# Performance work log

Measured on AMD Instinct MI355X. Metric: run time of the kernel, lower is better.

Reference implementation:

```python
import jax, jax.numpy as jnp
import numpy as np

B, L, D = 4, 2048, 512
H = 8
DK = 512 // H  # 64
DV = 512 // H  # 64
TEMP = float(np.power(DK, 0.5))
LN_EPS = 1e-5


def setup_inputs() -> dict:
    key = jax.random.key(0)
    ks = jax.random.split(key, 12)
    s = 0.02
    return {
        "q": jax.random.normal(ks[0], (B, L, D), jnp.float32),
        "k": jax.random.normal(ks[1], (B, L, D), jnp.float32),
        "v": jax.random.normal(ks[2], (B, L, D), jnp.float32),
        "mask": jax.random.randint(ks[3], (B, L, L), 0, 2, jnp.int32),
        "wq_w": jax.random.normal(ks[4], (H * DK, D), jnp.float32) * s,
        "wq_b": jnp.zeros((H * DK,), jnp.float32),
        "wv_w": jax.random.normal(ks[5], (H * DV, D), jnp.float32) * s,
        "wv_b": jnp.zeros((H * DV,), jnp.float32),
        "fc_w": jax.random.normal(ks[6], (D, H * DV), jnp.float32) * s,
        "fc_b": jnp.zeros((D,), jnp.float32),
        "ln_g": jnp.ones((D,), jnp.float32),
        "ln_b": jnp.zeros((D,), jnp.float32),
    }


def reference(q, k, v, mask, wq_w, wq_b, wv_w, wv_b, fc_w, fc_b, ln_g, ln_b):
    residual = q
    # NOTE: source module projects k with w_qs (bug preserved faithfully)
    qh = (q @ wq_w.T + wq_b).reshape(B, L, H, DK).transpose(0, 2, 1, 3)  # bhld
    kh = (k @ wq_w.T + wq_b).reshape(B, L, H, DK).transpose(0, 2, 1, 3)
    vh = (v @ wv_w.T + wv_b).reshape(B, L, H, DV).transpose(0, 2, 1, 3)
    attn = jnp.einsum("bhqd,bhkd->bhqk", qh / TEMP, kh)
    attn = jnp.where(mask[:, None, :, :] == 1, -1e9, attn)
    attn = jax.nn.softmax(attn, axis=-1)
    out = jnp.einsum("bhqk,bhkd->bhqd", attn, vh)  # (B, H, L, DV)
    # faithful buffer reinterpretation: .view(n_head, sz_b, L, DV)
    out = out.reshape(H, B, L, DV).transpose(0, 2, 1, 3).reshape(B, L, H * DV)
    out = out @ fc_w.T + fc_b
    x = out + residual
    mu = jnp.mean(x, axis=-1, keepdims=True)
    var = jnp.mean(jnp.square(x - mu), axis=-1, keepdims=True)
    y = (x - mu) / jnp.sqrt(var + LN_EPS) * ln_g + ln_b
    return (y, attn)
```

## Files before the change

kernel.cpp:

```cpp
#include <hip/hip_runtime.h>

#define NB 4
#define NL 2048
#define ND 512
#define NH 8
#define NTOK (NB * NL)

constexpr float LN_EPS = 1e-5f;

typedef __attribute__((ext_vector_type(8))) short bf16x8;
typedef __attribute__((ext_vector_type(4))) float f32x4;

static __device__ __forceinline__ unsigned short f2bf(float f) {
  unsigned u = __builtin_bit_cast(unsigned, f);
  unsigned r = (u + 0x7fffu + ((u >> 16) & 1u)) >> 16;
  return (unsigned short)r;
}

static __device__ __forceinline__ uint2 pk4(const float4 f) {
  uint2 r;
  r.x = (unsigned)f2bf(f.x) | ((unsigned)f2bf(f.y) << 16);
  r.y = (unsigned)f2bf(f.z) | ((unsigned)f2bf(f.w) << 16);
  return r;
}

#define MFMA_GEMM_PRELUDE                                                      \
  __shared__ unsigned short As[64 * 72];                                       \
  __shared__ unsigned short Bs[64 * 72];                                       \
  const int tid = threadIdx.x;                                                 \
  const int w = tid >> 6;                                                      \
  const int lane = tid & 63;                                                   \
  const int quad = lane >> 4, l15 = lane & 15;                                 \
  const int m0 = blockIdx.x * 64, n0 = blockIdx.y * 64;                        \
  const int srow = tid >> 2;                                                   \
  const int c4 = (tid & 3) * 4;                                                \
  const int scol = (tid & 3) * 16;                                             \
  f32x4 acc[4];                                                                \
  acc[0] = acc[1] = acc[2] = acc[3] = (f32x4){0.f, 0.f, 0.f, 0.f};

#define MFMA_STEP(AV, BV)                                                      \
  do {                                                                         \
    __syncthreads();                                                           \
    _Pragma("unroll") for (int j = 0; j < 4; ++j) {                            \
      *(uint2*)&As[srow * 72 + c4 + j * 16] = pk4(AV[j]);                      \
      *(uint2*)&Bs[srow * 72 + c4 + j * 16] = pk4(BV[j]);                      \
    }                                                                          \
    __syncthreads();                                                           \
    _Pragma("unroll") for (int ks = 0; ks < 2; ++ks) {                         \
      const bf16x8 af = *(const bf16x8*)&As[(w * 16 + l15) * 72 + ks * 32 + quad * 8]; \
      _Pragma("unroll") for (int nt = 0; nt < 4; ++nt) {                       \
        const bf16x8 bfr = *(const bf16x8*)&Bs[(nt * 16 + l15) * 72 + ks * 32 + quad * 8]; \
        acc[nt] = __builtin_amdgcn_mfma_f32_16x16x32_bf16(af, bfr, acc[nt], 0, 0, 0); \
      }                                                                        \
    }                                                                          \
  } while (0)

__global__ __launch_bounds__(256) void gemm_qk_mfma(const float* __restrict__ X,
                                                    const float* __restrict__ W,
                                                    const float* __restrict__ bias,
                                                    unsigned short* __restrict__ out,
                                                    float scale) {
  MFMA_GEMM_PRELUDE
  for (int k0 = 0; k0 < 512; k0 += 64) {
    float4 av[4], bv[4];
#pragma unroll
    for (int j = 0; j < 4; ++j) {
      av[j] = *(const float4*)&X[(size_t)(m0 + srow) * ND + k0 + c4 + j * 16];
      bv[j] = *(const float4*)&W[(size_t)(n0 + srow) * ND + k0 + c4 + j * 16];
    }
    MFMA_STEP(av, bv);
  }
  const int hh = n0 >> 6;
  __syncthreads();
#pragma unroll
  for (int nt = 0; nt < 4; ++nt) {
    const float b = bias[n0 + nt * 16 + l15];
#pragma unroll
    for (int r = 0; r < 4; ++r)
      As[(w * 16 + quad * 4 + r) * 72 + nt * 16 + l15] = f2bf((acc[nt][r] + b) * scale);
  }
  __syncthreads();
  const int tok = m0 + srow;
  const int bb = tok >> 11, l = tok & 2047;
  unsigned short* orow = out + (((size_t)bb * NH + hh) * NL + l) * 64;
  *(uint4*)&orow[scol] = *(const uint4*)&As[srow * 72 + scol];
  *(uint4*)&orow[scol + 8] = *(const uint4*)&As[srow * 72 + scol + 8];
}

__global__ __launch_bounds__(256) void gemm_v_mfma_t(const float* __restrict__ X,
                                                     const float* __restrict__ W,
                                                     const float* __restrict__ bias,
                                                     unsigned short* __restrict__ outT) {
  MFMA_GEMM_PRELUDE
  for (int k0 = 0; k0 < 512; k0 += 64) {
    float4 av[4], bv[4];
#pragma unroll
    for (int j = 0; j < 4; ++j) {
      av[j] = *(const float4*)&X[(size_t)(m0 + srow) * ND + k0 + c4 + j * 16];
      bv[j] = *(const float4*)&W[(size_t)(n0 + srow) * ND + k0 + c4 + j * 16];
    }
    MFMA_STEP(av, bv);
  }
  const int hh = n0 >> 6;
  __syncthreads();
#pragma unroll
  for (int nt = 0; nt < 4; ++nt) {
    const float b = bias[n0 + nt * 16 + l15];
#pragma unroll
    for (int r = 0; r < 4; ++r)
      As[(nt * 16 + l15) * 72 + w * 16 + quad * 4 + r] = f2bf(acc[nt][r] + b);
  }
  __syncthreads();
  const int bb = m0 >> 11, l0 = m0 & 2047;
  unsigned short* orow = outT + (((size_t)bb * NH + hh) * 64 + srow) * NL + l0;
  *(uint4*)&orow[scol] = *(const uint4*)&As[srow * 72 + scol];
  *(uint4*)&orow[scol + 8] = *(const uint4*)&As[srow * 72 + scol + 8];
}

__global__ __launch_bounds__(256) void attn_mfma(const unsigned short* __restrict__ qh,
                                                 const unsigned short* __restrict__ kh,
                                                 const unsigned short* __restrict__ vT,
                                                 const int* __restrict__ mask,
                                                 float* __restrict__ attn,
                                                 float* __restrict__ ao) {
  const int b = blockIdx.z, h = blockIdx.y, q0 = blockIdx.x * 64;
  const int bh = b * NH + h;
  __shared__ unsigned short Ks[64 * 72];
  __shared__ unsigned short Vt[64 * 72];
  __shared__ unsigned short Ps[4 * 16 * 72];
  const int tid = threadIdx.x;
  const int w = tid >> 6, lane = tid & 63;
  const int quad = lane >> 4, l15 = lane & 15;

  const size_t qoff = ((size_t)bh * NL + q0 + w * 16 + l15) * 64 + quad * 8;
  const bf16x8 aq0 = *(const bf16x8*)(qh + qoff);
  const bf16x8 aq1 = *(const bf16x8*)(qh + qoff + 32);

  const int srow = tid >> 2;
  const int scol = (tid & 3) * 16;

  float rinv[4] = {0.f, 0.f, 0.f, 0.f};
  unsigned int mbits[16];
#pragma unroll
  for (int i = 0; i < 16; ++i) mbits[i] = 0;

  for (int kt = 0; kt < 32; ++kt) {
    const unsigned short* kg = kh + ((size_t)bh * NL + kt * 64 + srow) * 64 + scol;
    const uint4 k0 = *(const uint4*)kg;
    const uint4 k1 = *(const uint4*)(kg + 8);
    __syncthreads();
    *(uint4*)&Ks[srow * 72 + scol] = k0;
    *(uint4*)&Ks[srow * 72 + scol + 8] = k1;
    __syncthreads();
    f32x4 s[4];
#pragma unroll
    for (int nt = 0; nt < 4; ++nt) {
      const bf16x8 b0 = *(const bf16x8*)&Ks[(nt * 16 + l15) * 72 + quad * 8];
      const bf16x8 b1 = *(const bf16x8*)&Ks[(nt * 16 + l15) * 72 + 32 + quad * 8];
      f32x4 acc = {0.f, 0.f, 0.f, 0.f};
      acc = __builtin_amdgcn_mfma_f32_16x16x32_bf16(aq0, b0, acc, 0, 0, 0);
      acc = __builtin_amdgcn_mfma_f32_16x16x32_bf16(aq1, b1, acc, 0, 0, 0);
      s[nt] = acc;
    }
    unsigned int mb = 0;
#pragma unroll
    for (int r = 0; r < 4; ++r) {
      const size_t mrow = ((size_t)b * NL + q0 + w * 16 + quad * 4 + r) * NL + kt * 64;
#pragma unroll
      for (int nt = 0; nt < 4; ++nt) {
        const int mz = mask[mrow + nt * 16 + l15];
        float e = __expf(s[nt][r]);
        if (mz == 1) {
          mb |= (1u << (nt * 4 + r));
          e = 0.f;
        }
        rinv[r] += e;
      }
    }
    mbits[kt >> 1] |= mb << ((kt & 1) * 16);
  }
#pragma unroll
  for (int r = 0; r < 4; ++r) {
    float v = rinv[r];
    v += __shfl_xor(v, 1);
    v += __shfl_xor(v, 2);
    v += __shfl_xor(v, 4);
    v += __shfl_xor(v, 8);
    rinv[r] = 1.0f / v;
  }

  f32x4 oacc[4];
#pragma unroll
  for (int nt = 0; nt < 4; ++nt) oacc[nt] = (f32x4){0.f, 0.f, 0.f, 0.f};

  for (int kt = 0; kt < 32; ++kt) {
    const unsigned short* kg = kh + ((size_t)bh * NL + kt * 64 + srow) * 64 + scol;
    const unsigned short* vg = vT + ((size_t)bh * 64 + srow) * NL + kt * 64 + scol;
    const uint4 k0 = *(const uint4*)kg;
    const uint4 k1 = *(const uint4*)(kg + 8);
    const uint4 v0 = *(const uint4*)vg;
    const uint4 v1 = *(const uint4*)(vg + 8);
    __syncthreads();
    *(uint4*)&Ks[srow * 72 + scol] = k0;
    *(uint4*)&Ks[srow * 72 + scol + 8] = k1;
    *(uint4*)&Vt[srow * 72 + scol] = v0;
    *(uint4*)&Vt[srow * 72 + scol + 8] = v1;
    __syncthreads();
    f32x4 s[4];
#pragma unroll
    for (int nt = 0; nt < 4; ++nt) {
      const bf16x8 b0 = *(const bf16x8*)&Ks[(nt * 16 + l15) * 72 + quad * 8];
      const bf16x8 b1 = *(const bf16x8*)&Ks[(nt * 16 + l15) * 72 + 32 + quad * 8];
      f32x4 acc = {0.f, 0.f, 0.f, 0.f};
      acc = __builtin_amdgcn_mfma_f32_16x16x32_bf16(aq0, b0, acc, 0, 0, 0);
      acc = __builtin_amdgcn_mfma_f32_16x16x32_bf16(aq1, b1, acc, 0, 0, 0);
      s[nt] = acc;
    }
    const unsigned int mb = mbits[kt >> 1] >> ((kt & 1) * 16);
#pragma unroll
    for (int r = 0; r < 4; ++r) {
      const int q = q0 + w * 16 + quad * 4 + r;
      float* arow = attn + ((size_t)bh * NL + q) * NL + kt * 64;
      unsigned short* prow = &Ps[(w * 16 + quad * 4 + r) * 72];
#pragma unroll
      for (int nt = 0; nt < 4; ++nt) {
        float e = ((mb >> (nt * 4 + r)) & 1u) ? 0.f : __expf(s[nt][r]) * rinv[r];
        arow[nt * 16 + l15] = e;
        prow[nt * 16 + l15] = f2bf(e);
      }
    }
    const bf16x8 pa0 = *(const bf16x8*)&Ps[(w * 16 + l15) * 72 + quad * 8];
    const bf16x8 pa1 = *(const bf16x8*)&Ps[(w * 16 + l15) * 72 + 32 + quad * 8];
#pragma unroll
    for (int nt = 0; nt < 4; ++nt) {
      const bf16x8 vb0 = *(const bf16x8*)&Vt[(nt * 16 + l15) * 72 + quad * 8];
      const bf16x8 vb1 = *(const bf16x8*)&Vt[(nt * 16 + l15) * 72 + 32 + quad * 8];
      oacc[nt] = __builtin_amdgcn_mfma_f32_16x16x32_bf16(pa0, vb0, oacc[nt], 0, 0, 0);
      oacc[nt] = __builtin_amdgcn_mfma_f32_16x16x32_bf16(pa1, vb1, oacc[nt], 0, 0, 0);
    }
  }
#pragma unroll
  for (int r = 0; r < 4; ++r) {
    float* orow = ao + ((size_t)bh * NL + q0 + w * 16 + quad * 4 + r) * 64;
#pragma unroll
    for (int nt = 0; nt < 4; ++nt) orow[nt * 16 + l15] = oacc[nt][r];
  }
}

__global__ __launch_bounds__(256) void fc_gather_mfma(const float* __restrict__ AO,
                                                      const float* __restrict__ W,
                                                      const float* __restrict__ bias,
                                                      const float* __restrict__ resid,
                                                      float* __restrict__ Xout) {
  MFMA_GEMM_PRELUDE
  const int nrow = m0 + srow;
  const int b_out = nrow >> 11;
  const int l_out = nrow & 2047;
  const int h2 = b_out * 2 + (l_out >> 10);
  const int q2base = (l_out & 1023) << 1;
  for (int k0 = 0; k0 < 512; k0 += 64) {
    const int q2 = q2base | ((k0 >> 8) & 1);
    const int b2 = (k0 >> 6) & 3;
    const float* abase = AO + ((size_t)(h2 * 4 + b2) * NL + q2) * 64;
    float4 av[4], bv[4];
#pragma unroll
    for (int j = 0; j < 4; ++j) {
      av[j] = *(const float4*)&abase[c4 + j * 16];
      bv[j] = *(const float4*)&W[(size_t)(n0 + srow) * ND + k0 + c4 + j * 16];
    }
    MFMA_STEP(av, bv);
  }
#pragma unroll
  for (int nt = 0; nt < 4; ++nt) {
    const float b = bias[n0 + nt * 16 + l15];
#pragma unroll
    for (int r = 0; r < 4; ++r) {
      const int row = m0 + w * 16 + quad * 4 + r;
      const float rv = resid[(size_t)row * ND + n0 + nt * 16 + l15];
      Xout[(size_t)row * ND + n0 + nt * 16 + l15] = acc[nt][r] + b + rv;
    }
  }
}

__global__ __launch_bounds__(64) void layernorm_k(const float* __restrict__ x,
                                                  const float* __restrict__ g,
                                                  const float* __restrict__ bta,
                                                  float* __restrict__ y) {
  const int n = blockIdx.x;
  const int lane = threadIdx.x;
  const float* row = x + (size_t)n * ND;
  const float4 a = *(const float4*)&row[lane * 8];
  const float4 c = *(const float4*)&row[lane * 8 + 4];
  float s = a.x + a.y + a.z + a.w + c.x + c.y + c.z + c.w;
  float sq = a.x * a.x + a.y * a.y + a.z * a.z + a.w * a.w +
             c.x * c.x + c.y * c.y + c.z * c.z + c.w * c.w;
#pragma unroll
  for (int off = 32; off; off >>= 1) {
    s += __shfl_down(s, off);
    sq += __shfl_down(sq, off);
  }
  s = __shfl(s, 0);
  sq = __shfl(sq, 0);
  const float mu = s * (1.f / 512.f);
  const float var = sq * (1.f / 512.f) - mu * mu;
  const float rstd = rsqrtf(var + LN_EPS);
  float* yo = y + (size_t)n * ND;
  const int c0 = lane * 8;
  float4 o1, o2;
  o1.x = (a.x - mu) * rstd * g[c0 + 0] + bta[c0 + 0];
  o1.y = (a.y - mu) * rstd * g[c0 + 1] + bta[c0 + 1];
  o1.z = (a.z - mu) * rstd * g[c0 + 2] + bta[c0 + 2];
  o1.w = (a.w - mu) * rstd * g[c0 + 3] + bta[c0 + 3];
  o2.x = (c.x - mu) * rstd * g[c0 + 4] + bta[c0 + 4];
  o2.y = (c.y - mu) * rstd * g[c0 + 5] + bta[c0 + 5];
  o2.z = (c.z - mu) * rstd * g[c0 + 6] + bta[c0 + 6];
  o2.w = (c.w - mu) * rstd * g[c0 + 7] + bta[c0 + 7];
  *(float4*)&yo[c0] = o1;
  *(float4*)&yo[c0 + 4] = o2;
}

extern "C" void kernel_launch(void* const* d_in, const int* in_sizes, int n_in,
                              void* d_out, int out_size, void* d_ws, size_t ws_size,
                              hipStream_t stream) {
  const float* q = (const float*)d_in[0];
  const float* k = (const float*)d_in[1];
  const float* v = (const float*)d_in[2];
  const int* mask = (const int*)d_in[3];
  const float* wq_w = (const float*)d_in[4];
  const float* wq_b = (const float*)d_in[5];
  const float* wv_w = (const float*)d_in[6];
  const float* wv_b = (const float*)d_in[7];
  const float* fc_w = (const float*)d_in[8];
  const float* fc_b = (const float*)d_in[9];
  const float* ln_g = (const float*)d_in[10];
  const float* ln_b = (const float*)d_in[11];

  float* y = (float*)d_out;
  float* attn = y + (size_t)NTOK * ND;

  const size_t SZ = (size_t)NTOK * ND;
  unsigned short* qhb = (unsigned short*)d_ws;
  unsigned short* khb = qhb + SZ;
  unsigned short* vTb = khb + SZ;
  float* ao = (float*)(vTb + SZ);
  float* xx = ao + SZ;

  const dim3 gproj(NTOK / 64, ND / 64);
  gemm_qk_mfma<<<gproj, 256, 0, stream>>>(q, wq_w, wq_b, qhb, 0.125f);
  gemm_qk_mfma<<<gproj, 256, 0, stream>>>(k, wq_w, wq_b, khb, 1.0f);
  gemm_v_mfma_t<<<gproj, 256, 0, stream>>>(v, wv_w, wv_b, vTb);
  attn_mfma<<<dim3(NL / 64, NH, NB), 256, 0, stream>>>(qhb, khb, vTb, mask, attn, ao);
  fc_gather_mfma<<<gproj, 256, 0, stream>>>(ao, fc_w, fc_b, q, xx);
  layernorm_k<<<NTOK, 64, 0, stream>>>(xx, ln_g, ln_b, y);
}
```

Measured before the change: 870.4 us.

## Pre-convert inputs and weights to bf16, bit-pack mask, store attention output as bf16

Adds a pre-pass that converts q/k/v and the three weight matrices to bf16, so the projection and fc GEMMs load bf16 directly instead of converting fp32 per tile. The int32 mask is packed into 64-bit ballot words once, so the attention kernel reads one 64-bit word per row per key tile rather than 64 int32 values. The attention output is also written as bf16 through shared memory with vectorized stores. The extra conversion kernels cost an additional read and write pass over the inputs, which may offset the savings.

```diff
diff --git a/kernel.cpp b/kernel.cpp
--- a/kernel.cpp
+++ b/kernel.cpp
@@ -24,7 +24,33 @@
   return r;
 }
 
-#define MFMA_GEMM_PRELUDE                                                      \
+__global__ __launch_bounds__(256) void cvt3_bf16(const float* __restrict__ s0,
+                                                 const float* __restrict__ s1,
+                                                 const float* __restrict__ s2,
+                                                 unsigned short* __restrict__ d0,
+                                                 unsigned short* __restrict__ d1,
+                                                 unsigned short* __restrict__ d2) {
+  const float* s = (blockIdx.y == 0) ? s0 : (blockIdx.y == 1) ? s1 : s2;
+  unsigned short* d = (blockIdx.y == 0) ? d0 : (blockIdx.y == 1) ? d1 : d2;
+  const size_t i = ((size_t)blockIdx.x * 256 + threadIdx.x) * 8;
+  const float4 a = *(const float4*)&s[i];
+  const float4 b = *(const float4*)&s[i + 4];
+  uint4 o;
+  const uint2 lo = pk4(a), hi = pk4(b);
+  o.x = lo.x; o.y = lo.y; o.z = hi.x; o.w = hi.y;
+  *(uint4*)&d[i] = o;
+}
+
+__global__ __launch_bounds__(256) void pack_mask(const int* __restrict__ mask,
+                                                 unsigned long long* __restrict__ mpk) {
+  const int w = threadIdx.x >> 6, lane = threadIdx.x & 63;
+  const size_t g = (size_t)blockIdx.x * 4 + w;
+  const int m = mask[g * 64 + lane];
+  const unsigned long long bits = __ballot(m == 1);
+  if (lane == 0) mpk[g] = bits;
+}
+
+#define BF16_GEMM_PRELUDE                                                      \
   __shared__ unsigned short As[64 * 72];                                       \
   __shared__ unsigned short Bs[64 * 72];                                       \
   const int tid = threadIdx.x;                                                 \
@@ -33,18 +59,21 @@
   const int quad = lane >> 4, l15 = lane & 15;                                 \
   const int m0 = blockIdx.x * 64, n0 = blockIdx.y * 64;                        \
   const int srow = tid >> 2;                                                   \
-  const int c4 = (tid & 3) * 4;                                                \
   const int scol = (tid & 3) * 16;                                             \
   f32x4 acc[4];                                                                \
   acc[0] = acc[1] = acc[2] = acc[3] = (f32x4){0.f, 0.f, 0.f, 0.f};
 
-#define MFMA_STEP(AV, BV)                                                      \
+#define BF16_GEMM_STEP(ap, bp)                                                 \
   do {                                                                         \
+    const uint4 a0 = *(const uint4*)((ap));                                    \
+    const uint4 a1 = *(const uint4*)((ap) + 8);                                \
+    const uint4 b0 = *(const uint4*)((bp));                                    \
+    const uint4 b1 = *(const uint4*)((bp) + 8);                                \
     __syncthreads();                                                           \
-    _Pragma("unroll") for (int j = 0; j < 4; ++j) {                            \
-      *(uint2*)&As[srow * 72 + c4 + j * 16] = pk4(AV[j]);                      \
-      *(uint2*)&Bs[srow * 72 + c4 + j * 16] = pk4(BV[j]);                      \
-    }                                                                          \
+    *(uint4*)&As[srow * 72 + scol] = a0;                                       \
+    *(uint4*)&As[srow * 72 + scol + 8] = a1;                                   \
+    *(uint4*)&Bs[srow * 72 + scol] = b0;                                       \
+    *(uint4*)&Bs[srow * 72 + scol + 8] = b1;                                   \
     __syncthreads();                                                           \
     _Pragma("unroll") for (int ks = 0; ks < 2; ++ks) {                         \
       const bf16x8 af = *(const bf16x8*)&As[(w * 16 + l15) * 72 + ks * 32 + quad * 8]; \
@@ -55,20 +84,16 @@
     }                                                                          \
   } while (0)
 
-__global__ __launch_bounds__(256) void gemm_qk_mfma(const float* __restrict__ X,
-                                                    const float* __restrict__ W,
+__global__ __launch_bounds__(256) void gemm_qk_mfma(const unsigned short* __restrict__ X,
+                                                    const unsigned short* __restrict__ W,
                                                     const float* __restrict__ bias,
                                                     unsigned short* __restrict__ out,
                                                     float scale) {
-  MFMA_GEMM_PRELUDE
+  BF16_GEMM_PRELUDE
   for (int k0 = 0; k0 < 512; k0 += 64) {
-    float4 av[4], bv[4];
-#pragma unroll
-    for (int j = 0; j < 4; ++j) {
-      av[j] = *(const float4*)&X[(size_t)(m0 + srow) * ND + k0 + c4 + j * 16];
-      bv[j] = *(const float4*)&W[(size_t)(n0 + srow) * ND + k0 + c4 + j * 16];
-    }
-    MFMA_STEP(av, bv);
+    const unsigned short* ap = X + (size_t)(m0 + srow) * ND + k0 + scol;
+    const unsigned short* bp = W + (size_t)(n0 + srow) * ND + k0 + scol;
+    BF16_GEMM_STEP(ap, bp);
   }
   const int hh = n0 >> 6;
   __syncthreads();
@@ -87,19 +112,15 @@
   *(uint4*)&orow[scol + 8] = *(const uint4*)&As[srow * 72 + scol + 8];
 }
 
-__global__ __launch_bounds__(256) void gemm_v_mfma_t(const float* __restrict__ X,
-                                                     const float* __restrict__ W,
+__global__ __launch_bounds__(256) void gemm_v_mfma_t(const unsigned short* __restrict__ X,
+                                                     const unsigned short* __restrict__ W,
                                                      const float* __restrict__ bias,
                                                      unsigned short* __restrict__ outT) {
-  MFMA_GEMM_PRELUDE
+  BF16_GEMM_PRELUDE
   for (int k0 = 0; k0 < 512; k0 += 64) {
-    float4 av[4], bv[4];
-#pragma unroll
-    for (int j = 0; j < 4; ++j) {
-      av[j] = *(const float4*)&X[(size_t)(m0 + srow) * ND + k0 + c4 + j * 16];
-      bv[j] = *(const float4*)&W[(size_t)(n0 + srow) * ND + k0 + c4 + j * 16];
-    }
-    MFMA_STEP(av, bv);
+    const unsigned short* ap = X + (size_t)(m0 + srow) * ND + k0 + scol;
+    const unsigned short* bp = W + (size_t)(n0 + srow) * ND + k0 + scol;
+    BF16_GEMM_STEP(ap, bp);
   }
   const int hh = n0 >> 6;
   __syncthreads();
@@ -120,9 +141,9 @@
 __global__ __launch_bounds__(256) void attn_mfma(const unsigned short* __restrict__ qh,
                                                  const unsigned short* __restrict__ kh,
                                                  const unsigned short* __restrict__ vT,
-                                                 const int* __restrict__ mask,
+                                                 const unsigned long long* __restrict__ mpk,
                                                  float* __restrict__ attn,
-                                                 float* __restrict__ ao) {
+                                                 unsigned short* __restrict__ ao) {
   const int b = blockIdx.z, h = blockIdx.y, q0 = blockIdx.x * 64;
   const int bh = b * NH + h;
   __shared__ unsigned short Ks[64 * 72];
@@ -139,6 +160,8 @@
   const int srow = tid >> 2;
   const int scol = (tid & 3) * 16;
 
+  const size_t mrowq = ((size_t)b * NL + q0 + w * 16 + quad * 4) * 32;
+
   float rinv[4] = {0.f, 0.f, 0.f, 0.f};
   unsigned int mbits[16];
 #pragma unroll
@@ -148,6 +171,9 @@
     const unsigned short* kg = kh + ((size_t)bh * NL + kt * 64 + srow) * 64 + scol;
     const uint4 k0 = *(const uint4*)kg;
     const uint4 k1 = *(const uint4*)(kg + 8);
+    unsigned long long mq[4];
+#pragma unroll
+    for (int r = 0; r < 4; ++r) mq[r] = mpk[mrowq + (size_t)r * 32 + kt];
     __syncthreads();
     *(uint4*)&Ks[srow * 72 + scol] = k0;
     *(uint4*)&Ks[srow * 72 + scol + 8] = k1;
@@ -165,15 +191,17 @@
     unsigned int mb = 0;
 #pragma unroll
     for (int r = 0; r < 4; ++r) {
-      const size_t mrow = ((size_t)b * NL + q0 + w * 16 + quad * 4 + r) * NL + kt * 64;
+      const unsigned long long t = mq[r] >> l15;
+      mb |= ((unsigned)t & 1u) << (0 + r);
+      mb |= (((unsigned)t >> 16) & 1u) << (4 + r);
+      mb |= (((unsigned)(t >> 32)) & 1u) << (8 + r);
+      mb |= (((unsigned)(t >> 48)) & 1u) << (12 + r);
+    }
+#pragma unroll
+    for (int r = 0; r < 4; ++r) {
 #pragma unroll
       for (int nt = 0; nt < 4; ++nt) {
-        const int mz = mask[mrow + nt * 16 + l15];
-        float e = __expf(s[nt][r]);
-        if (mz == 1) {
-          mb |= (1u << (nt * 4 + r));
-          e = 0.f;
-        }
+        const float e = ((mb >> (nt * 4 + r)) & 1u) ? 0.f : __expf(s[nt][r]);
         rinv[r] += e;
       }
     }
@@ -240,19 +268,23 @@
     }
   }
 #pragma unroll
-  for (int r = 0; r < 4; ++r) {
-    float* orow = ao + ((size_t)bh * NL + q0 + w * 16 + quad * 4 + r) * 64;
-#pragma unroll
-    for (int nt = 0; nt < 4; ++nt) orow[nt * 16 + l15] = oacc[nt][r];
-  }
-}
-
-__global__ __launch_bounds__(256) void fc_gather_mfma(const float* __restrict__ AO,
-                                                      const float* __restrict__ W,
+  for (int nt = 0; nt < 4; ++nt)
+#pragma unroll
+    for (int r = 0; r < 4; ++r)
+      Ps[(w * 16 + quad * 4 + r) * 72 + nt * 16 + l15] = f2bf(oacc[nt][r]);
+  const int erow = lane >> 2;
+  const int ecol = (lane & 3) * 16;
+  unsigned short* orow = ao + (((size_t)bh * NL + q0 + w * 16 + erow) * 64) + ecol;
+  *(uint4*)&orow[0] = *(const uint4*)&Ps[(w * 16 + erow) * 72 + ecol];
+  *(uint4*)&orow[8] = *(const uint4*)&Ps[(w * 16 + erow) * 72 + ecol + 8];
+}
+
+__global__ __launch_bounds__(256) void fc_gather_mfma(const unsigned short* __restrict__ AO,
+                                                      const unsigned short* __restrict__ W,
                                                       const float* __restrict__ bias,
                                                       const float* __restrict__ resid,
                                                       float* __restrict__ Xout) {
-  MFMA_GEMM_PRELUDE
+  BF16_GEMM_PRELUDE
   const int nrow = m0 + srow;
   const int b_out = nrow >> 11;
   const int l_out = nrow & 2047;
@@ -261,14 +293,9 @@
   for (int k0 = 0; k0 < 512; k0 += 64) {
     const int q2 = q2base | ((k0 >> 8) & 1);
     const int b2 = (k0 >> 6) & 3;
-    const float* abase = AO + ((size_t)(h2 * 4 + b2) * NL + q2) * 64;
-    float4 av[4], bv[4];
-#pragma unroll
-    for (int j = 0; j < 4; ++j) {
-      av[j] = *(const float4*)&abase[c4 + j * 16];
-      bv[j] = *(const float4*)&W[(size_t)(n0 + srow) * ND + k0 + c4 + j * 16];
-    }
-    MFMA_STEP(av, bv);
+    const unsigned short* ap = AO + ((size_t)(h2 * 4 + b2) * NL + q2) * 64 + scol;
+    const unsigned short* bp = W + (size_t)(n0 + srow) * ND + k0 + scol;
+    BF16_GEMM_STEP(ap, bp);
   }
 #pragma unroll
   for (int nt = 0; nt < 4; ++nt) {
@@ -339,17 +366,29 @@
   float* attn = y + (size_t)NTOK * ND;
 
   const size_t SZ = (size_t)NTOK * ND;
+  const size_t WSZ = (size_t)ND * ND;
   unsigned short* qhb = (unsigned short*)d_ws;
   unsigned short* khb = qhb + SZ;
   unsigned short* vTb = khb + SZ;
-  float* ao = (float*)(vTb + SZ);
-  float* xx = ao + SZ;
+  unsigned short* aob = vTb + SZ;
+  unsigned short* qb = aob + SZ;
+  unsigned short* kb = qb + SZ;
+  unsigned short* vb = kb + SZ;
+  float* xx = (float*)(vb + SZ);
+  unsigned short* wqb = (unsigned short*)(xx + SZ);
+  unsigned short* wvb = wqb + WSZ;
+  unsigned short* fcwb = wvb + WSZ;
+  unsigned long long* mpk = (unsigned long long*)(fcwb + WSZ);
+
+  cvt3_bf16<<<dim3(SZ / 2048, 3), 256, 0, stream>>>(q, k, v, qb, kb, vb);
+  cvt3_bf16<<<dim3(WSZ / 2048, 3), 256, 0, stream>>>(wq_w, wv_w, fc_w, wqb, wvb, fcwb);
+  pack_mask<<<(NB * NL * 32) / 4, 256, 0, stream>>>(mask, mpk);
 
   const dim3 gproj(NTOK / 64, ND / 64);
-  gemm_qk_mfma<<<gproj, 256, 0, stream>>>(q, wq_w, wq_b, qhb, 0.125f);
-  gemm_qk_mfma<<<gproj, 256, 0, stream>>>(k, wq_w, wq_b, khb, 1.0f);
-  gemm_v_mfma_t<<<gproj, 256, 0, stream>>>(v, wv_w, wv_b, vTb);
-  attn_mfma<<<dim3(NL / 64, NH, NB), 256, 0, stream>>>(qhb, khb, vTb, mask, attn, ao);
-  fc_gather_mfma<<<gproj, 256, 0, stream>>>(ao, fc_w, fc_b, q, xx);
+  gemm_qk_mfma<<<gproj, 256, 0, stream>>>(qb, wqb, wq_b, qhb, 0.125f);
+  gemm_qk_mfma<<<gproj, 256, 0, stream>>>(kb, wqb, wq_b, khb, 1.0f);
+  gemm_v_mfma_t<<<gproj, 256, 0, stream>>>(vb, wvb, wv_b, vTb);
+  attn_mfma<<<dim3(NL / 64, NH, NB), 256, 0, stream>>>(qhb, khb, vTb, mpk, attn, aob);
+  fc_gather_mfma<<<gproj, 256, 0, stream>>>(aob, fcwb, fc_b, q, xx);
   layernorm_k<<<NTOK, 64, 0, stream>>>(xx, ln_g, ln_b, y);
 }
```

Result: faster. 822.0 us (-5.6%).
